# Performance work log

Hardware: AMD Instinct MI355X
Metric: run time of the kernel (lower is better)

Reference implementation:

```python
import jax, jax.numpy as jnp
from jax import lax
import numpy as np

N = 128      # number of dictionary atoms (ConvTranspose in_channels)
K = 16       # kernel size
S = 8        # stride
R_LR = 0.1   # SGD lr on codes R
LMDA = 0.005 # soft-threshold level
MAX_ITER = 20  # cap on ISTA iterations (torch loop is uncapped)


def conv_t(R, W):
    """torch ConvTranspose2d(N,1,K,stride=S,bias=False) with weight W[N,1,K,K].
    Implemented as a fractionally-strided conv: transpose to OIHW and flip spatial."""
    Wt = jnp.flip(jnp.transpose(W, (1, 0, 2, 3)), axis=(2, 3))  # [1,N,K,K]
    return lax.conv_general_dilated(
        R, Wt,
        window_strides=(1, 1),
        padding=[(K - 1, K - 1), (K - 1, K - 1)],
        lhs_dilation=(S, S),
        dimension_numbers=("NCHW", "OIHW", "NCHW"),
    )  # [B,1,D,D] with D=(c-1)*S+K


def ista(img, W):
    B, D = img.shape[0], img.shape[2]
    c = (D - K) // S + 1
    R0 = jnp.zeros((B, N, c, c), img.dtype)

    loss_grad = jax.grad(lambda r: jnp.sum((img - conv_t(r, W)) ** 2))

    def cond(state):
        _, i, converged = state
        return jnp.logical_and(jnp.logical_not(converged), i < MAX_ITER)

    def body(state):
        R, i, _ = state
        g = loss_grad(R)                       # dL/dR
        Rn = R - R_LR * g                      # SGD step
        Rn = jax.nn.relu(Rn - LMDA) - jax.nn.relu(-Rn - LMDA)  # soft threshold
        converged = jnp.linalg.norm(Rn - R) / jnp.linalg.norm(R) < 0.01
        return (Rn, i + 1, converged)

    R, _, _ = lax.while_loop(cond, body, (R0, jnp.int32(0), jnp.bool_(False)))
    return R


def setup_inputs() -> dict:
    key = jax.random.key(0)
    k1, k2 = jax.random.split(key)
    img = jax.random.normal(k1, (128, 1, 128, 128), jnp.float32)
    W = jax.random.normal(k2, (N, 1, K, K), jnp.float32)
    # normalize_weights(): unit L2 norm per atom (flatten over out_ch,K,K)
    W = W / jnp.linalg.norm(W.reshape(N, -1), axis=1).reshape(N, 1, 1, 1)
    return {"img_batch": img, "U_weight": W}


def reference(img_batch, U_weight):
    R = ista(img_batch, U_weight)
    return conv_t(R, U_weight)
```

## Files before the change

### kernel.cpp

```cpp
#include <hip/hip_runtime.h>
#include <stdint.h>

#define BATCH 128
#define NAT   128
#define DIM   128
#define CP    17
#define MAXIT 20
#define STEP  0.2f
#define LMD   0.005f
#define NGRAD 900

typedef short bf16x8 __attribute__((ext_vector_type(8)));
typedef float f32x16 __attribute__((ext_vector_type(16)));

#define SZ_RP (BATCH*CP*CP*NAT)
#define SZ_RS (BATCH*DIM*DIM)
#define O_RP   0
#define O_RSH  (O_RP + SZ_RP*2)
#define O_W2H  (O_RSH + SZ_RS*2)
#define O_W2L  (O_W2H + 64*512*2)
#define O_WTH  (O_W2L + 64*512*2)
#define O_WTL  (O_WTH + 128*256*2)
#define O_PART (O_WTL + 128*256*2)

#define GLOAD16(gp, lp) __builtin_amdgcn_global_load_lds( \
    (const __attribute__((address_space(1))) uint32_t*)(gp), \
    (__attribute__((address_space(3))) uint32_t*)(lp), 16, 0, 0)

__device__ __forceinline__ void split2(float x, ushort& h, ushort& l) {
    uint32_t u = __float_as_uint(x);
    uint32_t hr = (u + 0x7FFFu + ((u >> 16) & 1u)) >> 16;
    h = (ushort)hr;
    float r = x - __uint_as_float(hr << 16);
    uint32_t u2 = __float_as_uint(r);
    l = (ushort)((u2 + 0x7FFFu + ((u2 >> 16) & 1u)) >> 16);
}
__device__ __forceinline__ float us2f(ushort u) {
    return __uint_as_float(((uint32_t)u) << 16);
}
__device__ __forceinline__ uint pk(ushort a, ushort b) {
    return (uint)a | ((uint)b << 16);
}
__device__ __forceinline__ ushort f2bf(float x) {
    uint32_t u = __float_as_uint(x);
    return (ushort)((u + 0x7FFFu + ((u >> 16) & 1u)) >> 16);
}

__global__ void kzero(uint4* __restrict__ rp) {
    int i = blockIdx.x * 256 + threadIdx.x;
    rp[i] = uint4{0u, 0u, 0u, 0u};
}

__global__ void kprep(const float* __restrict__ W,
                      ushort* __restrict__ wth, ushort* __restrict__ wtl,
                      ushort* __restrict__ w2h, ushort* __restrict__ w2l) {
    int tid = blockIdx.x * 256 + threadIdx.x;
    int n = tid >> 8, kk = tid & 255;
    ushort h, l; split2(W[tid], h, l);
    wth[tid] = h; wtl[tid] = l;
    int kx = kk >> 4, ky = kk & 15;
    int uv = (kx & 7) * 8 + (ky & 7);
    int k2 = ((kx >> 3) * 2 + (ky >> 3)) * 128 + n;
    w2h[uv * 512 + k2] = h; w2l[uv * 512 + k2] = l;
}

__global__ void kinit0(const float* __restrict__ img, ushort* __restrict__ rsh) {
    int t8 = (blockIdx.x * 256 + threadIdx.x) * 8;
    uint hw[4];
#pragma unroll
    for (int v = 0; v < 2; ++v) {
        float4 im = *(const float4*)&img[t8 + v * 4];
        hw[v*2+0] = pk(f2bf(im.x), f2bf(im.y));
        hw[v*2+1] = pk(f2bf(im.z), f2bf(im.w));
    }
    *(uint4*)&rsh[t8] = uint4{hw[0],hw[1],hw[2],hw[3]};
}

__global__ __launch_bounds__(256) void kconvt(
    const ushort* __restrict__ rp, const ushort* __restrict__ w2h,
    const float* __restrict__ img, ushort* __restrict__ rsh)
{
    const int tid = threadIdx.x;
    __shared__ uint4 lds[4096];
    const int bx = blockIdx.x;
    const int bid = ((bx & 7) << 6) | (bx >> 3);
    const int m0 = bid * 64;
    const int lane = tid & 63, w = tid >> 6;
    const int wm = w >> 1, wn = w & 1, g = lane >> 5;
    const int u = (lane & 7) ^ ((lane >> 3) & 7);

    const int b0 = m0 >> 8;
    const int x0 = ((m0 & 255) >> 4) * 8;
    const int erow = tid >> 3, ec0 = (tid & 7) * 16;
    const int ebase = b0 * DIM * DIM + (x0 + erow) * DIM + ec0;
    float4 im0 = *(const float4*)&img[ebase];
    float4 im1 = *(const float4*)&img[ebase + 4];
    float4 im2 = *(const float4*)&img[ebase + 8];
    float4 im3 = *(const float4*)&img[ebase + 12];
    __builtin_amdgcn_sched_barrier(0);

    int off0[4]; const ushort* srcp[4];
#pragma unroll
    for (int i = 0; i < 4; ++i) {
        int s = w * 4 + i;
        if (s < 8) {
            int ml = s * 8 + (lane >> 3);
            int mm = m0 + ml;
            int b_ = mm >> 8, cell = mm & 255, px0 = cell >> 4, py0 = cell & 15;
            off0[i] = ((b_ * CP + px0 + 1) * CP + py0 + 1) * NAT + u * 8;
            srcp[i] = rp;
        } else {
            int ml = (s - 8) * 8 + (lane >> 3);
            off0[i] = ml * 512 + u * 8;
            srcp[i] = w2h;
        }
    }
    auto stage = [&](int kc, int buf) {
        int ij = kc >> 1;
        int dA = (kc & 1) * 64 - ((ij >> 1) * CP + (ij & 1)) * NAT;
        int dB = kc * 64;
        uint4* base = lds + buf * 1024;
#pragma unroll
        for (int i = 0; i < 4; ++i) {
            int s = w * 4 + i;
            GLOAD16(srcp[i] + off0[i] + (s < 8 ? dA : dB), base + s * 64);
        }
    };

    f32x16 acc = {};
    const int arow = wm * 32 + (lane & 31);
    const int brow = wn * 32 + (lane & 31);
    const int ax = lane & 7;

    stage(0, 0); stage(1, 1); stage(2, 2);
    for (int kc = 0; kc < 8; ++kc) {
        if (kc < 5) stage(kc + 3, (kc + 3) & 3);
        int nf = 7 - kc; nf = nf > 3 ? 3 : nf;
        switch (nf) {
            case 3: asm volatile("s_waitcnt vmcnt(12)" ::: "memory"); break;
            case 2: asm volatile("s_waitcnt vmcnt(8)"  ::: "memory"); break;
            case 1: asm volatile("s_waitcnt vmcnt(4)"  ::: "memory"); break;
            default: asm volatile("s_waitcnt vmcnt(0)" ::: "memory"); break;
        }
        __builtin_amdgcn_s_barrier();
        __builtin_amdgcn_sched_barrier(0);
        const uint4* Lb = lds + (kc & 3) * 1024;
#pragma unroll
        for (int ks = 0; ks < 4; ++ks) {
            int un = (ks * 2 + g) ^ ax;
            bf16x8 Ah = __builtin_bit_cast(bf16x8, Lb[      arow * 8 + un]);
            bf16x8 Bh = __builtin_bit_cast(bf16x8, Lb[512 + brow * 8 + un]);
            acc = __builtin_amdgcn_mfma_f32_32x32x16_bf16(Ah, Bh, acc, 0, 0, 0);
        }
        __builtin_amdgcn_sched_barrier(0);
        __builtin_amdgcn_s_barrier();
    }

    float* ldsO = (float*)lds;
    const int uvx = wn * 32 + (lane & 31);
    const int uu = uvx >> 3, vv = uvx & 7;
#pragma unroll
    for (int r = 0; r < 16; ++r) {
        int mr = m0 + wm * 32 + (r & 3) + 8 * (r >> 2) + 4 * g;
        int cl = mr & 255;
        ldsO[(((cl >> 4) & 3) * 8 + uu) * 129 + (cl & 15) * 8 + vv] = acc[r];
    }
    __syncthreads();
    const float* lrow = &ldsO[erow * 129 + ec0];
    uint hw[8];
    hw[0] = pk(f2bf(im0.x - lrow[0]),  f2bf(im0.y - lrow[1]));
    hw[1] = pk(f2bf(im0.z - lrow[2]),  f2bf(im0.w - lrow[3]));
    hw[2] = pk(f2bf(im1.x - lrow[4]),  f2bf(im1.y - lrow[5]));
    hw[3] = pk(f2bf(im1.z - lrow[6]),  f2bf(im1.w - lrow[7]));
    hw[4] = pk(f2bf(im2.x - lrow[8]),  f2bf(im2.y - lrow[9]));
    hw[5] = pk(f2bf(im2.z - lrow[10]), f2bf(im2.w - lrow[11]));
    hw[6] = pk(f2bf(im3.x - lrow[12]), f2bf(im3.y - lrow[13]));
    hw[7] = pk(f2bf(im3.z - lrow[14]), f2bf(im3.w - lrow[15]));
    *(uint4*)&rsh[ebase]     = uint4{hw[0],hw[1],hw[2],hw[3]};
    *(uint4*)&rsh[ebase + 8] = uint4{hw[4],hw[5],hw[6],hw[7]};
}

__global__ __launch_bounds__(256) void kgrad(
    const ushort* __restrict__ rsh, const ushort* __restrict__ wth,
    ushort* __restrict__ rp, float* __restrict__ partials, int t)
{
    __shared__ uint4 lds[3072];
    __shared__ float red0[16];
    __shared__ int sg;
    const int tid = threadIdx.x;
    const int bx = blockIdx.x;
    const int xcd = bx & 7;
    const int bid = (xcd < 2 ? xcd * 57 : 114 + (xcd - 2) * 56) + (bx >> 3);
    const int m0 = bid * 64;
    const int n0 = blockIdx.y * 64;
    const int lane = tid & 63, w = tid >> 6;
    const int wm = w >> 1, wn = w & 1, g = lane >> 5;
    const int u = (lane & 7) ^ ((lane >> 3) & 7);
    const int pb2 = blockIdx.y * 450 + bid;
    const float* bankO = partials + ((t - 1) & 1) * 2048;
    float* bankN = partials + (t & 1) * 2048;

    float gd[4] = {0.f, 0.f, 0.f, 0.f}, gr[4] = {0.f, 0.f, 0.f, 0.f};
    float pod = 0.f, por = 0.f;
    if (t >= 1) {
#pragma unroll
        for (int k = 0; k < 4; ++k) {
            int i = tid + k * 256;
            if (i < NGRAD) { gd[k] = bankO[i]; gr[k] = bankO[1024 + i]; }
        }
        pod = bankO[pb2]; por = bankO[1024 + pb2];
    }
    int rbase0, rbase1; uint4 rv0, rv1;
    {
        int item = tid;
        int rowL = item >> 3, ch = item & 7;
        int mr = m0 + rowL;
        int bb = mr / 225, rm = mr % 225, pxx = rm / 15, pyy = rm % 15;
        rbase0 = ((bb * CP + pxx + 1) * CP + pyy + 1) * NAT + n0 + ch * 8;
        rv0 = *(const uint4*)&rp[rbase0];
    }
    {
        int item = 256 + tid;
        int rowL = item >> 3, ch = item & 7;
        int mr = m0 + rowL;
        int bb = mr / 225, rm = mr % 225, pxx = rm / 15, pyy = rm % 15;
        rbase1 = ((bb * CP + pxx + 1) * CP + pyy + 1) * NAT + n0 + ch * 8;
        rv1 = *(const uint4*)&rp[rbase1];
    }
    __builtin_amdgcn_sched_barrier(0);

    int off0[4]; const ushort* srcp[4];
#pragma unroll
    for (int i = 0; i < 4; ++i) {
        int s = w * 4 + i;
        if (s < 8) {
            int ml = s * 8 + (lane >> 3);
            int mA = m0 + ml, bA = mA / 225, rm = mA % 225, px = rm / 15, py = rm % 15;
            off0[i] = bA * DIM * DIM + (8 * px + (u >> 1)) * DIM + 8 * py + (u & 1) * 8;
            srcp[i] = rsh;
        } else {
            int ml = (s - 8) * 8 + (lane >> 3);
            off0[i] = (n0 + ml) * 256 + u * 8;
            srcp[i] = wth;
        }
    }
    auto stage = [&](int kc, int buf) {
        uint4* base = lds + buf * 1024;
#pragma unroll
        for (int i = 0; i < 4; ++i) {
            int s = w * 4 + i;
            GLOAD16(srcp[i] + off0[i] + (s < 8 ? kc * 512 : kc * 64), base + s * 64);
        }
    };

    f32x16 acc = {};
    const int arow = wm * 32 + (lane & 31);
    const int brow = wn * 32 + (lane & 31);
    const int ax = lane & 7;

    stage(0, 0); stage(1, 1);
    for (int kc = 0; kc < 4; ++kc) {
        if (kc < 2) stage(kc + 2, (kc + 2) % 3);
        int nf = 3 - kc; nf = nf > 2 ? 2 : nf;
        switch (nf) {
            case 2: asm volatile("s_waitcnt vmcnt(8)" ::: "memory"); break;
            case 1: asm volatile("s_waitcnt vmcnt(4)" ::: "memory"); break;
            default: asm volatile("s_waitcnt vmcnt(0)" ::: "memory"); break;
        }
        __builtin_amdgcn_s_barrier();
        __builtin_amdgcn_sched_barrier(0);
        const uint4* Lb = lds + (kc % 3) * 1024;
#pragma unroll
        for (int ks = 0; ks < 4; ++ks) {
            int un = (ks * 2 + g) ^ ax;
            bf16x8 Ah = __builtin_bit_cast(bf16x8, Lb[      arow * 8 + un]);
            bf16x8 Bh = __builtin_bit_cast(bf16x8, Lb[512 + brow * 8 + un]);
            acc = __builtin_amdgcn_mfma_f32_32x32x16_bf16(Ah, Bh, acc, 0, 0, 0);
        }
        __builtin_amdgcn_sched_barrier(0);
        __builtin_amdgcn_s_barrier();
    }

    int gate = 0;
    if (t >= 1) {
        float d2 = 0.f, r2 = 0.f;
        d2 += gd[0]; d2 += gd[1]; d2 += gd[2]; d2 += gd[3];
        r2 += gr[0]; r2 += gr[1]; r2 += gr[2]; r2 += gr[3];
        for (int off = 32; off; off >>= 1) { d2 += __shfl_down(d2, off, 64); r2 += __shfl_down(r2, off, 64); }
        int w_ = tid >> 6, l = tid & 63;
        if (l == 0) { red0[w_] = d2; red0[8 + w_] = r2; }
        __syncthreads();
        if (tid == 0) {
            float td = red0[0] + red0[1] + red0[2] + red0[3];
            float tr = red0[8] + red0[9] + red0[10] + red0[11];
            sg = (td < 1e-4f * tr) ? 1 : 0;
        }
        __syncthreads();
        gate = sg;
    }
    const bool dow = (t == 0) || (gate == 0);

    float* ldsO = (float*)lds;
    {
        const int colL = wn * 32 + (lane & 31);
#pragma unroll
        for (int r = 0; r < 16; ++r) {
            int rowL = wm * 32 + (r & 3) + 8 * (r >> 2) + 4 * g;
            ldsO[rowL * 76 + colL] = acc[r];
        }
    }
    __syncthreads();

    float d2 = 0.f, r2 = 0.f;
    if (dow) {
#pragma unroll
        for (int i = 0; i < 2; ++i) {
            int item = i * 256 + tid;
            int rowL = item >> 3, ch = item & 7;
            uint4 hv = i ? rv1 : rv0;
            int base = i ? rbase1 : rbase0;
            const float* lp = &ldsO[rowL * 76 + ch * 8];
            uint ho[4];
#pragma unroll
            for (int wd = 0; wd < 4; ++wd) {
                uint hw_ = ((const uint*)&hv)[wd];
                ushort nh0, nh1;
                {
                    float rold = us2f((ushort)hw_);
                    float v = fmaf(STEP, lp[wd * 2 + 0], rold);
                    float st = fmaxf(v - LMD, 0.f) - fmaxf(-v - LMD, 0.f);
                    nh0 = f2bf(st);
                    float df = us2f(nh0) - rold;
                    d2 += df * df; r2 += rold * rold;
                }
                {
                    float rold = us2f((ushort)(hw_ >> 16));
                    float v = fmaf(STEP, lp[wd * 2 + 1], rold);
                    float st = fmaxf(v - LMD, 0.f) - fmaxf(-v - LMD, 0.f);
                    nh1 = f2bf(st);
                    float df = us2f(nh1) - rold;
                    d2 += df * df; r2 += rold * rold;
                }
                ho[wd] = pk(nh0, nh1);
            }
            *(uint4*)&rp[base] = uint4{ho[0], ho[1], ho[2], ho[3]};
        }
    }

    for (int off = 32; off; off >>= 1) { d2 += __shfl_down(d2, off, 64); r2 += __shfl_down(r2, off, 64); }
    int w_ = tid >> 6, l = tid & 63;
    if (l == 0) { red0[w_] = d2; red0[8 + w_] = r2; }
    __syncthreads();
    if (tid == 0) {
        if (dow) {
            float td = red0[0] + red0[1] + red0[2] + red0[3];
            float tr = red0[8] + red0[9] + red0[10] + red0[11];
            bankN[pb2] = td;
            bankN[1024 + pb2] = tr;
        } else {
            bankN[pb2] = pod;
            bankN[1024 + pb2] = por;
        }
    }
}

__global__ __launch_bounds__(256) void kfinal(
    const ushort* __restrict__ rp,
    const ushort* __restrict__ w2h, const ushort* __restrict__ w2l,
    float* __restrict__ outp)
{
    const int tid = threadIdx.x;
    __shared__ uint4 lds[3072];
    const int bx = blockIdx.x;
    const int bid = ((bx & 7) << 6) | (bx >> 3);
    const int m0 = bid * 64;
    const int lane = tid & 63, w = tid >> 6;
    const int wm = w >> 1, wn = w & 1, g = lane >> 5;
    const int u = (lane & 7) ^ ((lane >> 3) & 7);

    const ushort* const srcs[3] = {rp, w2h, w2l};
    int off0[6]; const ushort* srcp[6];
#pragma unroll
    for (int i = 0; i < 6; ++i) {
        int j = w * 6 + i, p = j >> 3, jj = j & 7;
        int ml = jj * 8 + (lane >> 3);
        srcp[i] = srcs[p];
        if (p == 0) {
            int mm = m0 + ml;
            int b_ = mm >> 8, cell = mm & 255, px0 = cell >> 4, py0 = cell & 15;
            off0[i] = ((b_ * CP + px0 + 1) * CP + py0 + 1) * NAT + u * 8;
        } else {
            off0[i] = ml * 512 + u * 8;
        }
    }
    auto stage = [&](int kc, int buf) {
        int ij = kc >> 1;
        int dA = (kc & 1) * 64 - ((ij >> 1) * CP + (ij & 1)) * NAT;
        int dB = kc * 64;
#pragma unroll
        for (int i = 0; i < 6; ++i) {
            int j = w * 6 + i;
            GLOAD16(srcp[i] + off0[i] + (j < 8 ? dA : dB), lds + buf * 1536 + j * 64);
        }
    };

    f32x16 acc = {};
    const int arow = wm * 32 + (lane & 31);
    const int brow = wn * 32 + (lane & 31);
    const int ax = lane & 7;

    stage(0, 0);
    __syncthreads();
    for (int kc = 0;; ++kc) {
        const int cur = kc & 1;
        if (kc < 7) stage(kc + 1, cur ^ 1);
        const uint4* Lb = lds + cur * 1536;
#pragma unroll
        for (int ks = 0; ks < 4; ++ks) {
            int un = (ks * 2 + g) ^ ax;
            bf16x8 Ah = __builtin_bit_cast(bf16x8, Lb[       arow * 8 + un]);
            bf16x8 Bh = __builtin_bit_cast(bf16x8, Lb[512  + brow * 8 + un]);
            bf16x8 Bl = __builtin_bit_cast(bf16x8, Lb[1024 + brow * 8 + un]);
            acc = __builtin_amdgcn_mfma_f32_32x32x16_bf16(Ah, Bh, acc, 0, 0, 0);
            acc = __builtin_amdgcn_mfma_f32_32x32x16_bf16(Ah, Bl, acc, 0, 0, 0);
        }
        if (kc == 7) break;
        __syncthreads();
    }

    __syncthreads();
    float* ldsO = (float*)lds;
    const int uvx = wn * 32 + (lane & 31);
    const int uu = uvx >> 3, vv = uvx & 7;
#pragma unroll
    for (int r = 0; r < 16; ++r) {
        int mr = m0 + wm * 32 + (r & 3) + 8 * (r >> 2) + 4 * g;
        int cl = mr & 255;
        ldsO[(((cl >> 4) & 3) * 8 + uu) * 129 + (cl & 15) * 8 + vv] = acc[r];
    }
    __syncthreads();
    const int b0 = m0 >> 8;
    const int x0 = ((m0 & 255) >> 4) * 8;
    const int row = tid >> 3, c0 = (tid & 7) * 16;
    const int base = b0 * DIM * DIM + (x0 + row) * DIM + c0;
    const float* lrow = &ldsO[row * 129 + c0];
#pragma unroll
    for (int v = 0; v < 4; ++v)
        *(float4*)&outp[base + v * 4] =
            float4{lrow[v*4], lrow[v*4+1], lrow[v*4+2], lrow[v*4+3]};
}

extern "C" void kernel_launch(void* const* d_in, const int* in_sizes, int n_in,
                              void* d_out, int out_size, void* d_ws, size_t ws_size,
                              hipStream_t stream) {
    const float* img = (const float*)d_in[0];
    const float* W   = (const float*)d_in[1];
    char* ws = (char*)d_ws;
    ushort* rp  = (ushort*)(ws + O_RP);
    ushort* rsh = (ushort*)(ws + O_RSH);
    ushort* w2h = (ushort*)(ws + O_W2H);
    ushort* w2l = (ushort*)(ws + O_W2L);
    ushort* wth = (ushort*)(ws + O_WTH);
    ushort* wtl = (ushort*)(ws + O_WTL);
    float* partials = (float*)(ws + O_PART);
    float* outp = (float*)d_out;

    kzero<<<2312, 256, 0, stream>>>((uint4*)(ws + O_RP));
    kprep<<<128, 256, 0, stream>>>(W, wth, wtl, w2h, w2l);
    kinit0<<<1024, 256, 0, stream>>>(img, rsh);
    kgrad<<<dim3(450, 2), 256, 0, stream>>>(rsh, wth, rp, partials, 0);
    for (int t = 1; t < MAXIT; ++t) {
        kconvt<<<512, 256, 0, stream>>>(rp, w2h, img, rsh);
        kgrad<<<dim3(450, 2), 256, 0, stream>>>(rsh, wth, rp, partials, t);
    }
    kfinal<<<512, 256, 0, stream>>>(rp, w2h, w2l, outp);
}
```

Before: 431.8 us.

## Split kconvt K-loop across two wave groups with LDS reduction

Doubles kconvt block size to 512 threads. The two halves of the waves each process alternate K chunks of the 8-step MFMA loop, then combine their accumulators through LDS before the epilogue. The goal is more latency hiding and more parallel work per block on this small 64x64 tile GEMM. In exchange it adds an LDS exchange, an extra barrier, and a denser staging schedule in which all four buffers are filled up front.

```diff
diff --git a/kernel.cpp b/kernel.cpp
--- a/kernel.cpp
+++ b/kernel.cpp
@@ -76,7 +76,7 @@
     *(uint4*)&rsh[t8] = uint4{hw[0],hw[1],hw[2],hw[3]};
 }
 
-__global__ __launch_bounds__(256) void kconvt(
+__global__ __launch_bounds__(512, 4) void kconvt(
     const ushort* __restrict__ rp, const ushort* __restrict__ w2h,
     const float* __restrict__ img, ushort* __restrict__ rsh)
 {
@@ -86,23 +86,22 @@
     const int bid = ((bx & 7) << 6) | (bx >> 3);
     const int m0 = bid * 64;
     const int lane = tid & 63, w = tid >> 6;
-    const int wm = w >> 1, wn = w & 1, g = lane >> 5;
+    const int q = w & 3, h = w >> 2;
+    const int wm = q >> 1, wn = q & 1, g = lane >> 5;
     const int u = (lane & 7) ^ ((lane >> 3) & 7);
 
     const int b0 = m0 >> 8;
     const int x0 = ((m0 & 255) >> 4) * 8;
-    const int erow = tid >> 3, ec0 = (tid & 7) * 16;
+    const int erow = tid >> 4, ec0 = (tid & 15) * 8;
     const int ebase = b0 * DIM * DIM + (x0 + erow) * DIM + ec0;
     float4 im0 = *(const float4*)&img[ebase];
     float4 im1 = *(const float4*)&img[ebase + 4];
-    float4 im2 = *(const float4*)&img[ebase + 8];
-    float4 im3 = *(const float4*)&img[ebase + 12];
     __builtin_amdgcn_sched_barrier(0);
 
-    int off0[4]; const ushort* srcp[4];
-#pragma unroll
-    for (int i = 0; i < 4; ++i) {
-        int s = w * 4 + i;
+    int off0[2]; const ushort* srcp[2];
+#pragma unroll
+    for (int i = 0; i < 2; ++i) {
+        int s = w * 2 + i;
         if (s < 8) {
             int ml = s * 8 + (lane >> 3);
             int mm = m0 + ml;
@@ -121,8 +120,8 @@
         int dB = kc * 64;
         uint4* base = lds + buf * 1024;
 #pragma unroll
-        for (int i = 0; i < 4; ++i) {
-            int s = w * 4 + i;
+        for (int i = 0; i < 2; ++i) {
+            int s = w * 2 + i;
             GLOAD16(srcp[i] + off0[i] + (s < 8 ? dA : dB), base + s * 64);
         }
     };
@@ -132,19 +131,15 @@
     const int brow = wn * 32 + (lane & 31);
     const int ax = lane & 7;
 
-    stage(0, 0); stage(1, 1); stage(2, 2);
-    for (int kc = 0; kc < 8; ++kc) {
-        if (kc < 5) stage(kc + 3, (kc + 3) & 3);
-        int nf = 7 - kc; nf = nf > 3 ? 3 : nf;
-        switch (nf) {
-            case 3: asm volatile("s_waitcnt vmcnt(12)" ::: "memory"); break;
-            case 2: asm volatile("s_waitcnt vmcnt(8)"  ::: "memory"); break;
-            case 1: asm volatile("s_waitcnt vmcnt(4)"  ::: "memory"); break;
-            default: asm volatile("s_waitcnt vmcnt(0)" ::: "memory"); break;
-        }
+    stage(0, 0); stage(1, 1); stage(2, 2); stage(3, 3);
+    for (int s4 = 0; s4 < 4; ++s4) {
+        if (s4 == 1)      { stage(4, 0); stage(5, 1); }
+        else if (s4 == 2) { stage(6, 2); stage(7, 3); }
+        if (s4 < 3) asm volatile("s_waitcnt vmcnt(4)" ::: "memory");
+        else        asm volatile("s_waitcnt vmcnt(0)" ::: "memory");
         __builtin_amdgcn_s_barrier();
         __builtin_amdgcn_sched_barrier(0);
-        const uint4* Lb = lds + (kc & 3) * 1024;
+        const uint4* Lb = lds + ((2 * s4 + h) & 3) * 1024;
 #pragma unroll
         for (int ks = 0; ks < 4; ++ks) {
             int un = (ks * 2 + g) ^ ax;
@@ -156,28 +151,35 @@
         __builtin_amdgcn_s_barrier();
     }
 
-    float* ldsO = (float*)lds;
-    const int uvx = wn * 32 + (lane & 31);
-    const int uu = uvx >> 3, vv = uvx & 7;
-#pragma unroll
-    for (int r = 0; r < 16; ++r) {
-        int mr = m0 + wm * 32 + (r & 3) + 8 * (r >> 2) + 4 * g;
-        int cl = mr & 255;
-        ldsO[(((cl >> 4) & 3) * 8 + uu) * 129 + (cl & 15) * 8 + vv] = acc[r];
+    float* xch  = (float*)lds;
+    float* ldsO = (float*)lds + 8192;
+    if (h == 0) {
+#pragma unroll
+        for (int f = 0; f < 16; ++f)
+            xch[f * 256 + q * 64 + lane] = acc[f];
+    }
+    __syncthreads();
+    if (h == 1) {
+#pragma unroll
+        for (int f = 0; f < 16; ++f)
+            acc[f] += xch[f * 256 + q * 64 + lane];
+        const int uvx = wn * 32 + (lane & 31);
+        const int uu = uvx >> 3, vv = uvx & 7;
+#pragma unroll
+        for (int r = 0; r < 16; ++r) {
+            int mr = m0 + wm * 32 + (r & 3) + 8 * (r >> 2) + 4 * g;
+            int cl = mr & 255;
+            ldsO[(((cl >> 4) & 3) * 8 + uu) * 129 + (cl & 15) * 8 + vv] = acc[r];
+        }
     }
     __syncthreads();
     const float* lrow = &ldsO[erow * 129 + ec0];
-    uint hw[8];
-    hw[0] = pk(f2bf(im0.x - lrow[0]),  f2bf(im0.y - lrow[1]));
-    hw[1] = pk(f2bf(im0.z - lrow[2]),  f2bf(im0.w - lrow[3]));
-    hw[2] = pk(f2bf(im1.x - lrow[4]),  f2bf(im1.y - lrow[5]));
-    hw[3] = pk(f2bf(im1.z - lrow[6]),  f2bf(im1.w - lrow[7]));
-    hw[4] = pk(f2bf(im2.x - lrow[8]),  f2bf(im2.y - lrow[9]));
-    hw[5] = pk(f2bf(im2.z - lrow[10]), f2bf(im2.w - lrow[11]));
-    hw[6] = pk(f2bf(im3.x - lrow[12]), f2bf(im3.y - lrow[13]));
-    hw[7] = pk(f2bf(im3.z - lrow[14]), f2bf(im3.w - lrow[15]));
-    *(uint4*)&rsh[ebase]     = uint4{hw[0],hw[1],hw[2],hw[3]};
-    *(uint4*)&rsh[ebase + 8] = uint4{hw[4],hw[5],hw[6],hw[7]};
+    uint hw[4];
+    hw[0] = pk(f2bf(im0.x - lrow[0]), f2bf(im0.y - lrow[1]));
+    hw[1] = pk(f2bf(im0.z - lrow[2]), f2bf(im0.w - lrow[3]));
+    hw[2] = pk(f2bf(im1.x - lrow[4]), f2bf(im1.y - lrow[5]));
+    hw[3] = pk(f2bf(im1.z - lrow[6]), f2bf(im1.w - lrow[7]));
+    *(uint4*)&rsh[ebase] = uint4{hw[0], hw[1], hw[2], hw[3]};
 }
 
 __global__ __launch_bounds__(256) void kgrad(
@@ -470,7 +472,7 @@
     kinit0<<<1024, 256, 0, stream>>>(img, rsh);
     kgrad<<<dim3(450, 2), 256, 0, stream>>>(rsh, wth, rp, partials, 0);
     for (int t = 1; t < MAXIT; ++t) {
-        kconvt<<<512, 256, 0, stream>>>(rp, w2h, img, rsh);
+        kconvt<<<512, 512, 0, stream>>>(rp, w2h, img, rsh);
         kgrad<<<dim3(450, 2), 256, 0, stream>>>(rsh, wth, rp, partials, t);
     }
     kfinal<<<512, 256, 0, stream>>>(rp, w2h, w2l, outp);
```

Result: no change. 432.4 us (+0.1%).
